# Optimization experiments

Hardware: AMD Instinct MI355X
Metric: run time of the kernel (lower is better)

Reference implementation:

```python
import jax, jax.numpy as jnp
import numpy as np

FEATS = 1024
HEAD = 16
MLP_HIDDEN = 4096
B, N = 8, 1024
EPS = 1e-5


def _layernorm(x, g, b):
    mu = jnp.mean(x, axis=-1, keepdims=True)
    var = jnp.var(x, axis=-1, keepdims=True)
    return (x - mu) * jax.lax.rsqrt(var + EPS) * g + b


def setup_inputs() -> dict:
    key = jax.random.key(0)
    ks = jax.random.split(key, 12)
    s_attn = 1.0 / np.sqrt(FEATS)
    s_mlp1 = 1.0 / np.sqrt(FEATS)
    s_mlp2 = 1.0 / np.sqrt(MLP_HIDDEN)
    return {
        "x": jax.random.normal(ks[0], (B, N, FEATS), dtype=jnp.float32),
        "ln1_g": jnp.ones((FEATS,), jnp.float32),
        "ln1_b": jnp.zeros((FEATS,), jnp.float32),
        "wq": jax.random.normal(ks[1], (FEATS, FEATS), jnp.float32) * s_attn,
        "bq": jnp.zeros((FEATS,), jnp.float32),
        "wk": jax.random.normal(ks[2], (FEATS, FEATS), jnp.float32) * s_attn,
        "bk": jnp.zeros((FEATS,), jnp.float32),
        "wv": jax.random.normal(ks[3], (FEATS, FEATS), jnp.float32) * s_attn,
        "bv": jnp.zeros((FEATS,), jnp.float32),
        "wo": jax.random.normal(ks[4], (FEATS, FEATS), jnp.float32) * s_attn,
        "bo": jnp.zeros((FEATS,), jnp.float32),
        "ln2_g": jnp.ones((FEATS,), jnp.float32),
        "ln2_b": jnp.zeros((FEATS,), jnp.float32),
        "w1": jax.random.normal(ks[5], (FEATS, MLP_HIDDEN), jnp.float32) * s_mlp1,
        "b1": jnp.zeros((MLP_HIDDEN,), jnp.float32),
        "w2": jax.random.normal(ks[6], (MLP_HIDDEN, FEATS), jnp.float32) * s_mlp2,
        "b2": jnp.zeros((FEATS,), jnp.float32),
    }


def reference(x, ln1_g, ln1_b, wq, bq, wk, bk, wv, bv, wo, bo,
              ln2_g, ln2_b, w1, b1, w2, b2):
    b, n, f = x.shape
    d = f // HEAD
    sqrt_d = jnp.asarray(f, x.dtype) ** 0.5  # NOTE: scale by sqrt(feats), as in source

    h = _layernorm(x, ln1_g, ln1_b)
    # [b, n, f] -> [b, head, n, d]
    q = (h @ wq + bq).reshape(b, n, HEAD, d).transpose(0, 2, 1, 3)
    k = (h @ wk + bk).reshape(b, n, HEAD, d).transpose(0, 2, 1, 3)
    v = (h @ wv + bv).reshape(b, n, HEAD, d).transpose(0, 2, 1, 3)

    score = jnp.einsum('bhif,bhjf->bhij', q, k) / sqrt_d
    p = jax.nn.softmax(score, axis=-1)
    attn = jnp.einsum('bhij,bhjf->bihf', p, v).reshape(b, n, f)
    o = attn @ wo + bo
    out = o + x

    h2 = _layernorm(out, ln2_g, ln2_b)
    m = jax.nn.gelu(h2 @ w1 + b1, approximate=False)
    m = jax.nn.gelu(m @ w2 + b2, approximate=False)
    return m + out
```

## Files before the change

kernel.cpp:

```cpp
#include <hip/hip_runtime.h>
#include <cstdint>

typedef __bf16 bf16;
typedef __attribute__((ext_vector_type(8))) __bf16 bf16x8;
typedef __attribute__((ext_vector_type(4))) __bf16 bf16x4;
typedef __attribute__((ext_vector_type(4))) float f32x4;
typedef __attribute__((ext_vector_type(8))) unsigned short u16x8;

#define AS1C(p) ((const __attribute__((address_space(1))) void*)(p))
#define AS3(p)  ((__attribute__((address_space(3))) void*)(p))

__device__ __forceinline__ float gelu_exact(float v) {
    return 0.5f * v * (1.0f + erff(v * 0.7071067811865476f));
}

__global__ __launch_bounds__(256, 1) void wtrans_kernel(
    const float* __restrict__ w, bf16* __restrict__ wt, int K, int N)
{
    __shared__ float tile[64][65];
    const int k0 = blockIdx.y * 64, n0 = blockIdx.x * 64;
    const int tid = threadIdx.x;
    {
        const int kl = tid >> 2, nc = (tid & 3) * 16;
        #pragma unroll
        for (int i = 0; i < 4; ++i) {
            const float4 v = *(const float4*)&w[(size_t)(k0 + kl) * N + n0 + nc + i * 4];
            tile[kl][nc + i * 4 + 0] = v.x;
            tile[kl][nc + i * 4 + 1] = v.y;
            tile[kl][nc + i * 4 + 2] = v.z;
            tile[kl][nc + i * 4 + 3] = v.w;
        }
    }
    __syncthreads();
    {
        const int nl = tid >> 2, kc = (tid & 3) * 16;
        #pragma unroll
        for (int i = 0; i < 4; ++i) {
            bf16x4 o4;
            o4[0] = (bf16)tile[kc + i * 4 + 0][nl];
            o4[1] = (bf16)tile[kc + i * 4 + 1][nl];
            o4[2] = (bf16)tile[kc + i * 4 + 2][nl];
            o4[3] = (bf16)tile[kc + i * 4 + 3][nl];
            *(bf16x4*)&wt[(size_t)(n0 + nl) * K + k0 + kc + i * 4] = o4;
        }
    }
}

__global__ void bias3_kernel(const float* __restrict__ a, const float* __restrict__ b,
                             const float* __restrict__ c, float* __restrict__ o)
{
    const int i = blockIdx.x * 256 + threadIdx.x;
    o[i] = (i < 1024) ? a[i] : (i < 2048 ? b[i - 1024] : c[i - 2048]);
}

__global__ __launch_bounds__(256, 1) void ln_kernel(
    const float* __restrict__ x, const float* __restrict__ gw,
    const float* __restrict__ bw, bf16* __restrict__ out)
{
    const int row = blockIdx.x, tid = threadIdx.x;
    const float4 v = *(const float4*)&x[(size_t)row * 1024 + tid * 4];
    float s = v.x + v.y + v.z + v.w;
    float q = v.x * v.x + v.y * v.y + v.z * v.z + v.w * v.w;
    #pragma unroll
    for (int off = 32; off > 0; off >>= 1) {
        s += __shfl_xor(s, off);
        q += __shfl_xor(q, off);
    }
    __shared__ float red[8];
    if ((tid & 63) == 0) { red[tid >> 6] = s; red[4 + (tid >> 6)] = q; }
    __syncthreads();
    s = red[0] + red[1] + red[2] + red[3];
    q = red[4] + red[5] + red[6] + red[7];
    const float mu = s * (1.f / 1024.f);
    const float rs = rsqrtf(q * (1.f / 1024.f) - mu * mu + 1e-5f);
    const float4 gg = *(const float4*)&gw[tid * 4];
    const float4 bb = *(const float4*)&bw[tid * 4];
    bf16x4 o4;
    o4[0] = (bf16)((v.x - mu) * rs * gg.x + bb.x);
    o4[1] = (bf16)((v.y - mu) * rs * gg.y + bb.y);
    o4[2] = (bf16)((v.z - mu) * rs * gg.z + bb.z);
    o4[3] = (bf16)((v.w - mu) * rs * gg.w + bb.w);
    *(bf16x4*)&out[(size_t)row * 1024 + tid * 4] = o4;
}

template<int EPI>
__global__ __launch_bounds__(512, 2) void gemm_v10_kernel(
    const bf16* __restrict__ A, const bf16* __restrict__ BT,
    const float* __restrict__ bias, const float* __restrict__ res,
    void* __restrict__ out, int M, int N, int Kstride, int Klen)
{
    constexpr int ABYTES = 256 * 128;
    constexpr int BUFB = 512 * 128;
    extern __shared__ char lds[];

    const int tid = threadIdx.x;
    const int lane = tid & 63, wid = tid >> 6;
    const int wr = wid >> 2, wc = wid & 3;
    const int j = lane & 15, g = lane >> 4;
    const int skc = ((tid & 7) ^ ((tid >> 4) & 7)) << 3;

    const int nbn = N >> 8;
    const int nwg = (M >> 8) * nbn;
    const int wg = (blockIdx.x & 7) * ((int)gridDim.x >> 3) + (blockIdx.x >> 3);
    const int half = wg / nwg;
    const int wgl = wg - half * nwg;
    const int bm = (wgl / nbn) << 8;
    const int bn = (wgl % nbn) << 8;
    const int kbase = half * Klen;

    const bf16* srcA[4];
    const bf16* srcB[4];
    #pragma unroll
    for (int ga = 0; ga < 4; ++ga)
        srcA[ga] = A + (size_t)(bm + ga * 64 + (tid >> 3)) * Kstride + kbase + skc;
    #pragma unroll
    for (int gb = 0; gb < 4; ++gb)
        srcB[gb] = BT + (size_t)(bn + gb * 64 + (tid >> 3)) * Kstride + kbase + skc;

    auto stage = [&](char* obuf) {
        #pragma unroll
        for (int ga = 0; ga < 4; ++ga) {
            __builtin_amdgcn_global_load_lds(AS1C(srcA[ga]), AS3(obuf + ga * 8192 + tid * 16), 16, 0, 0);
            srcA[ga] += 64;
        }
        #pragma unroll
        for (int gb = 0; gb < 4; ++gb) {
            __builtin_amdgcn_global_load_lds(AS1C(srcB[gb]), AS3(obuf + ABYTES + gb * 8192 + tid * 16), 16, 0, 0);
            srcB[gb] += 64;
        }
    };
    auto rdA = [&](char* buf, int h, int mf, int ks) {
        const int R = wr * 128 + (h * 4 + mf) * 16 + j;
        uint32_t lb = (uint32_t)(R * 128 + ks * 64 + g * 16);
        lb ^= (lb >> 4) & 0x70u;
        return *(const bf16x8*)(buf + lb);
    };
    auto rdB = [&](char* buf, int nf, int ks) {
        const int R = wc * 64 + nf * 16 + j;
        uint32_t lb = (uint32_t)(R * 128 + ks * 64 + g * 16);
        lb ^= (lb >> 4) & 0x70u;
        return *(const bf16x8*)(buf + ABYTES + lb);
    };

    f32x4 acc[8][4] = {};
    const int NT = Klen >> 6;

    stage(lds);
    asm volatile("s_waitcnt vmcnt(0)" ::: "memory");
    __builtin_amdgcn_s_barrier();

    for (int t = 0; t < NT; ++t) {
        char* buf = lds + (t & 1) * BUFB;

        bf16x8 bfr[4][2], af[4][2];
        #pragma unroll
        for (int nf = 0; nf < 4; ++nf)
            #pragma unroll
            for (int ks = 0; ks < 2; ++ks) bfr[nf][ks] = rdB(buf, nf, ks);
        #pragma unroll
        for (int mf = 0; mf < 4; ++mf)
            #pragma unroll
            for (int ks = 0; ks < 2; ++ks) af[mf][ks] = rdA(buf, 0, mf, ks);
        if (t + 1 < NT) stage(lds + ((t + 1) & 1) * BUFB);
        __builtin_amdgcn_sched_barrier(0);
        __builtin_amdgcn_s_setprio(1);
        #pragma unroll
        for (int mf = 0; mf < 4; ++mf)
            #pragma unroll
            for (int nf = 0; nf < 4; ++nf)
                #pragma unroll
                for (int ks = 0; ks < 2; ++ks)
                    acc[mf][nf] = __builtin_amdgcn_mfma_f32_16x16x32_bf16(
                        af[mf][ks], bfr[nf][ks], acc[mf][nf], 0, 0, 0);
        __builtin_amdgcn_s_setprio(0);
        bf16x8 af1[4][2];
        #pragma unroll
        for (int mf = 0; mf < 4; ++mf)
            #pragma unroll
            for (int ks = 0; ks < 2; ++ks) af1[mf][ks] = rdA(buf, 1, mf, ks);
        __builtin_amdgcn_sched_barrier(0);
        __builtin_amdgcn_s_setprio(1);
        #pragma unroll
        for (int mf = 0; mf < 4; ++mf)
            #pragma unroll
            for (int nf = 0; nf < 4; ++nf)
                #pragma unroll
                for (int ks = 0; ks < 2; ++ks)
                    acc[4 + mf][nf] = __builtin_amdgcn_mfma_f32_16x16x32_bf16(
                        af1[mf][ks], bfr[nf][ks], acc[4 + mf][nf], 0, 0, 0);
        __builtin_amdgcn_s_setprio(0);
        asm volatile("s_waitcnt vmcnt(0)" ::: "memory");
        __builtin_amdgcn_s_barrier();
    }

    const int row0 = bm + wr * 128;
    const int col0 = bn + wc * 64;
    float* po = nullptr;
    if constexpr (EPI == 4)
        po = half ? (float*)res : (float*)out;
    #pragma unroll
    for (int nf = 0; nf < 4; ++nf) {
        const int col = col0 + nf * 16 + j;
        const float bs = (EPI == 4) ? 0.f : bias[col];
        #pragma unroll
        for (int mf = 0; mf < 8; ++mf) {
            #pragma unroll
            for (int r = 0; r < 4; ++r) {
                const int row = row0 + mf * 16 + g * 4 + r;
                float v = acc[mf][nf][r] + bs;
                if constexpr (EPI == 4) {
                    po[(size_t)row * N + col] = v;
                } else if constexpr (EPI == 2) {
                    ((bf16*)out)[(size_t)row * N + col] = (bf16)gelu_exact(v);
                } else if constexpr (EPI == 1) {
                    v += res[(size_t)row * N + col];
                    ((float*)out)[(size_t)row * N + col] = v;
                } else {
                    ((bf16*)out)[(size_t)row * N + col] = (bf16)v;
                }
            }
        }
    }
}

__global__ __launch_bounds__(256, 1) void reduce2_kernel(
    const float* __restrict__ p0, const float* __restrict__ p1,
    const float* __restrict__ bias, const float* __restrict__ res,
    float* __restrict__ out)
{
    const size_t i4 = ((size_t)blockIdx.x * 256 + threadIdx.x) * 4;
    const float4 a = *(const float4*)&p0[i4];
    const float4 b = *(const float4*)&p1[i4];
    const float4 r = *(const float4*)&res[i4];
    const float4 bs = *(const float4*)&bias[i4 & 1023];
    float4 o;
    o.x = gelu_exact(a.x + b.x + bs.x) + r.x;
    o.y = gelu_exact(a.y + b.y + bs.y) + r.y;
    o.z = gelu_exact(a.z + b.z + bs.z) + r.z;
    o.w = gelu_exact(a.w + b.w + bs.w) + r.w;
    *(float4*)&out[i4] = o;
}

__global__ __launch_bounds__(256, 1) void attn_kernel(
    const bf16* __restrict__ qkv, bf16* __restrict__ attn, int bh_base)
{
    const int tid = threadIdx.x;
    const int lane = tid & 63, wid = tid >> 6;
    const int j = lane & 15, g = lane >> 4;

    const int lin = blockIdx.x + blockIdx.y * 8;
    const int virt = (lin & 7) * 64 + (lin >> 3);
    const int bh = bh_base + (virt >> 3), qp = virt & 7;
    const int b = bh >> 4, h = bh & 15;
    const int q0a = qp * 128 + wid * 16;
    const int q0b = q0a + 64;

    const bf16* Qp = qkv + (size_t)b * 1024 * 3072 + h * 64;
    const bf16* Kp = Qp + 1024;
    const bf16* Vp = Qp + 2048;

    __shared__ __attribute__((aligned(16))) uint32_t vTu[4][64][36];

    const int kp = (tid & 31) * 2;
    const int d0 = (tid >> 5) * 8;
    #pragma unroll
    for (int pb = 0; pb < 2; ++pb) {
        const u16x8 r0 = *(const u16x8*)&Vp[(size_t)(pb * 64 + kp) * 3072 + d0];
        const u16x8 r1 = *(const u16x8*)&Vp[(size_t)(pb * 64 + kp + 1) * 3072 + d0];
        #pragma unroll
        for (int i = 0; i < 8; ++i)
            vTu[pb][d0 + i][kp >> 1] = (uint32_t)r0[i] | ((uint32_t)r1[i] << 16);
    }

    bf16x8 qa0 = *(const bf16x8*)&Qp[(size_t)(q0a + j) * 3072 + g * 8];
    bf16x8 qa1 = *(const bf16x8*)&Qp[(size_t)(q0a + j) * 3072 + 32 + g * 8];
    bf16x8 qb0 = *(const bf16x8*)&Qp[(size_t)(q0b + j) * 3072 + g * 8];
    bf16x8 qb1 = *(const bf16x8*)&Qp[(size_t)(q0b + j) * 3072 + 32 + g * 8];
    #pragma unroll
    for (int e = 0; e < 8; ++e) {
        qa0[e] = (bf16)((float)qa0[e] * 0.03125f);
        qa1[e] = (bf16)((float)qa1[e] * 0.03125f);
        qb0[e] = (bf16)((float)qb0[e] * 0.03125f);
        qb1[e] = (bf16)((float)qb1[e] * 0.03125f);
    }

    const int jperm = (j >> 2) * 8 + (j & 3);

    f32x4 oa[4] = {}, ob[4] = {};
    float mra = -1e30f, lsa = 0.f;
    float mrb = -1e30f, lsb = 0.f;

    bf16x8 kfA[4][2], kfB[4][2];
    #pragma unroll
    for (int t = 0; t < 4; ++t) {
        const int key = (t >> 1) * 32 + jperm + (t & 1) * 4;
        kfA[t][0] = *(const bf16x8*)&Kp[(size_t)key * 3072 + g * 8];
        kfA[t][1] = *(const bf16x8*)&Kp[(size_t)key * 3072 + 32 + g * 8];
    }

    asm volatile("s_waitcnt lgkmcnt(0)" ::: "memory");
    __builtin_amdgcn_s_barrier();

    auto softmax = [&](f32x4 (&s)[4], float& mrun, float& lsum, f32x4 (&o)[4]) {
        float cur = fmaxf(fmaxf(s[0][0], s[0][1]), fmaxf(s[0][2], s[0][3]));
        #pragma unroll
        for (int t = 1; t < 4; ++t)
            cur = fmaxf(cur, fmaxf(fmaxf(s[t][0], s[t][1]), fmaxf(s[t][2], s[t][3])));
        cur = fmaxf(cur, __shfl_xor(cur, 16));
        cur = fmaxf(cur, __shfl_xor(cur, 32));
        if (!__all(cur - mrun <= 8.0f)) {
            const float mnew = fmaxf(mrun, cur);
            const float alpha = __expf(mrun - mnew);
            float al[4];
            #pragma unroll
            for (int r = 0; r < 4; ++r) al[r] = __shfl(alpha, g * 4 + r);
            #pragma unroll
            for (int dt = 0; dt < 4; ++dt)
                #pragma unroll
                for (int r = 0; r < 4; ++r) o[dt][r] *= al[r];
            lsum *= alpha;
            mrun = mnew;
        }
        float ps = 0.f;
        #pragma unroll
        for (int t = 0; t < 4; ++t)
            #pragma unroll
            for (int r = 0; r < 4; ++r) {
                const float p = __expf(s[t][r] - mrun);
                s[t][r] = p;
                ps += p;
            }
        lsum += ps;
    };

    auto iter = [&](int c, bf16x8 (&kf)[4][2], bf16x8 (&kfn)[4][2]) {
        const f32x4 zero = {0.f, 0.f, 0.f, 0.f};
        const bool pfv = (c + 2 < 16);
        const bool pfk = (c + 1 < 16);

        u16x8 r0, r1;
        if (pfv) {
            const size_t vb = (size_t)((c + 2) * 64 + kp) * 3072 + d0;
            r0 = *(const u16x8*)&Vp[vb];
            r1 = *(const u16x8*)&Vp[vb + 3072];
        }

        f32x4 sa[4], sb[4];
        #pragma unroll
        for (int t = 0; t < 4; ++t) {
            sa[t] = __builtin_amdgcn_mfma_f32_16x16x32_bf16(kf[t][0], qa0, zero, 0, 0, 0);
            sb[t] = __builtin_amdgcn_mfma_f32_16x16x32_bf16(kf[t][0], qb0, zero, 0, 0, 0);
            sa[t] = __builtin_amdgcn_mfma_f32_16x16x32_bf16(kf[t][1], qa1, sa[t], 0, 0, 0);
            sb[t] = __builtin_amdgcn_mfma_f32_16x16x32_bf16(kf[t][1], qb1, sb[t], 0, 0, 0);
        }

        if (pfk) {
            #pragma unroll
            for (int t = 0; t < 4; ++t) {
                const int key = (c + 1) * 64 + (t >> 1) * 32 + jperm + (t & 1) * 4;
                kfn[t][0] = *(const bf16x8*)&Kp[(size_t)key * 3072 + g * 8];
                kfn[t][1] = *(const bf16x8*)&Kp[(size_t)key * 3072 + 32 + g * 8];
            }
        }

        softmax(sa, mra, lsa, oa);
        softmax(sb, mrb, lsb, ob);

        bf16x8 paa0, paa1, pab0, pab1;
        #pragma unroll
        for (int r = 0; r < 4; ++r) {
            paa0[r]     = (bf16)sa[0][r];
            paa0[4 + r] = (bf16)sa[1][r];
            paa1[r]     = (bf16)sa[2][r];
            paa1[4 + r] = (bf16)sa[3][r];
            pab0[r]     = (bf16)sb[0][r];
            pab0[4 + r] = (bf16)sb[1][r];
            pab1[r]     = (bf16)sb[2][r];
            pab1[4 + r] = (bf16)sb[3][r];
        }

        if (pfv) {
            const int wb = (c + 2) & 3;
            #pragma unroll
            for (int i = 0; i < 8; ++i)
                vTu[wb][d0 + i][kp >> 1] = (uint32_t)r0[i] | ((uint32_t)r1[i] << 16);
        }

        const int rb = c & 3;
        #pragma unroll
        for (int dt = 0; dt < 4; ++dt) {
            const bf16* vrow = (const bf16*)&vTu[rb][dt * 16 + j][0];
            const bf16x8 vb0 = *(const bf16x8*)(vrow + g * 8);
            const bf16x8 vb1 = *(const bf16x8*)(vrow + 32 + g * 8);
            oa[dt] = __builtin_amdgcn_mfma_f32_16x16x32_bf16(paa0, vb0, oa[dt], 0, 0, 0);
            ob[dt] = __builtin_amdgcn_mfma_f32_16x16x32_bf16(pab0, vb0, ob[dt], 0, 0, 0);
            oa[dt] = __builtin_amdgcn_mfma_f32_16x16x32_bf16(paa1, vb1, oa[dt], 0, 0, 0);
            ob[dt] = __builtin_amdgcn_mfma_f32_16x16x32_bf16(pab1, vb1, ob[dt], 0, 0, 0);
        }
    };

    for (int cc = 0; cc < 16; cc += 2) {
        iter(cc,     kfA, kfB);
        iter(cc + 1, kfB, kfA);
        asm volatile("s_waitcnt lgkmcnt(0)" ::: "memory");
        __builtin_amdgcn_sched_barrier(0);
        __builtin_amdgcn_s_barrier();
    }

    lsa += __shfl_xor(lsa, 16);
    lsa += __shfl_xor(lsa, 32);
    lsb += __shfl_xor(lsb, 16);
    lsb += __shfl_xor(lsb, 32);
    float inva[4], invb[4];
    #pragma unroll
    for (int r = 0; r < 4; ++r) {
        inva[r] = 1.0f / __shfl(lsa, g * 4 + r);
        invb[r] = 1.0f / __shfl(lsb, g * 4 + r);
    }
    #pragma unroll
    for (int dt = 0; dt < 4; ++dt)
        #pragma unroll
        for (int r = 0; r < 4; ++r) {
            attn[(size_t)(b * 1024 + q0a + g * 4 + r) * 1024 + h * 64 + dt * 16 + j] =
                (bf16)(oa[dt][r] * inva[r]);
            attn[(size_t)(b * 1024 + q0b + g * 4 + r) * 1024 + h * 64 + dt * 16 + j] =
                (bf16)(ob[dt][r] * invb[r]);
        }
}

extern "C" void kernel_launch(void* const* d_in, const int* in_sizes, int n_in,
                              void* d_out, int out_size, void* d_ws, size_t ws_size,
                              hipStream_t stream)
{
    const float* x    = (const float*)d_in[0];
    const float* ln1g = (const float*)d_in[1];
    const float* ln1b = (const float*)d_in[2];
    const float* wq   = (const float*)d_in[3];
    const float* bq   = (const float*)d_in[4];
    const float* wk   = (const float*)d_in[5];
    const float* bk   = (const float*)d_in[6];
    const float* wv   = (const float*)d_in[7];
    const float* bv   = (const float*)d_in[8];
    const float* wo   = (const float*)d_in[9];
    const float* bo   = (const float*)d_in[10];
    const float* ln2g = (const float*)d_in[11];
    const float* ln2b = (const float*)d_in[12];
    const float* w1   = (const float*)d_in[13];
    const float* b1   = (const float*)d_in[14];
    const float* w2   = (const float*)d_in[15];
    const float* b2   = (const float*)d_in[16];

    char* ws = (char*)d_ws;
    bf16* wqkvT = (bf16*)ws;  ws += (size_t)3072 * 1024 * 2;
    bf16* woT   = (bf16*)ws;  ws += (size_t)1024 * 1024 * 2;
    bf16* w1T   = (bf16*)ws;  ws += (size_t)4096 * 1024 * 2;
    bf16* w2T   = (bf16*)ws;  ws += (size_t)1024 * 4096 * 2;
    float* bqkv = (float*)ws; ws += (size_t)3072 * 4;
    bf16* h     = (bf16*)ws;  ws += (size_t)8192 * 1024 * 2;
    bf16* qkv   = (bf16*)ws;  ws += (size_t)8192 * 3072 * 2;
    bf16* attn  = (bf16*)ws;  ws += (size_t)8192 * 1024 * 2;
    float* outf = (float*)ws; ws += (size_t)8192 * 1024 * 4;
    bf16* m1    = (bf16*)ws;  ws += (size_t)8192 * 4096 * 2;
    float* p1   = (float*)ws; ws += (size_t)8192 * 1024 * 4;
    float* p0   = (float*)qkv;

    (void)hipFuncSetAttribute((const void*)gemm_v10_kernel<0>,
                              hipFuncAttributeMaxDynamicSharedMemorySize, 131072);
    (void)hipFuncSetAttribute((const void*)gemm_v10_kernel<1>,
                              hipFuncAttributeMaxDynamicSharedMemorySize, 131072);
    (void)hipFuncSetAttribute((const void*)gemm_v10_kernel<2>,
                              hipFuncAttributeMaxDynamicSharedMemorySize, 131072);
    (void)hipFuncSetAttribute((const void*)gemm_v10_kernel<4>,
                              hipFuncAttributeMaxDynamicSharedMemorySize, 131072);

    wtrans_kernel<<<dim3(16, 16), 256, 0, stream>>>(wq, wqkvT,                   1024, 1024);
    wtrans_kernel<<<dim3(16, 16), 256, 0, stream>>>(wk, wqkvT + 1024 * 1024,     1024, 1024);
    wtrans_kernel<<<dim3(16, 16), 256, 0, stream>>>(wv, wqkvT + 2 * 1024 * 1024, 1024, 1024);
    wtrans_kernel<<<dim3(16, 16), 256, 0, stream>>>(wo, woT, 1024, 1024);
    wtrans_kernel<<<dim3(64, 16), 256, 0, stream>>>(w1, w1T, 1024, 4096);
    wtrans_kernel<<<dim3(16, 64), 256, 0, stream>>>(w2, w2T, 4096, 1024);
    bias3_kernel<<<12, 256, 0, stream>>>(bq, bk, bv, bqkv);

    ln_kernel<<<8192, 256, 0, stream>>>(x, ln1g, ln1b, h);
    gemm_v10_kernel<0><<<384, 512, 131072, stream>>>(h, wqkvT, bqkv, nullptr, qkv, 8192, 3072, 1024, 1024);
    attn_kernel<<<dim3(8, 64), 256, 0, stream>>>(qkv, attn, 0);
    attn_kernel<<<dim3(8, 64), 256, 0, stream>>>(qkv, attn, 64);
    gemm_v10_kernel<1><<<128, 512, 131072, stream>>>(attn, woT, bo, x, outf, 8192, 1024, 1024, 1024);
    ln_kernel<<<8192, 256, 0, stream>>>(outf, ln2g, ln2b, h);
    gemm_v10_kernel<2><<<512, 512, 131072, stream>>>(h, w1T, b1, nullptr, m1, 8192, 4096, 1024, 1024);
    gemm_v10_kernel<4><<<256, 512, 131072, stream>>>(m1, w2T, nullptr, p1, p0, 8192, 1024, 4096, 2048);
    reduce2_kernel<<<8192, 256, 0, stream>>>(p0, p1, b2, outf, (float*)d_out);
}
```

Baseline: 449.4 us.

## Replace 256x256 pipelined GEMM with simple 128x128 single-buffered tiles

Swaps the double-buffered 256x256-tile, 512-thread GEMM for a 128x128-tile, 256-thread kernel. It uses a K step of 32, a single LDS buffer with no swizzle, and two barriers per iteration. The output-projection GEMM now uses split-K with a separate reduction pass, the reduce kernel gains a non-GELU mode, and the other launches grow their grids to match the smaller tiles. The aim is more workgroups and higher occupancy, at the cost of losing load/compute overlap, adding LDS bank conflicts, doing less data reuse per tile, and making an extra memory pass.

```diff
diff --git a/kernel.cpp b/kernel.cpp
--- a/kernel.cpp
+++ b/kernel.cpp
@@ -84,130 +84,70 @@
 }
 
 template<int EPI>
-__global__ __launch_bounds__(512, 2) void gemm_v10_kernel(
+__global__ __launch_bounds__(256, 3) void gemm_v11_kernel(
     const bf16* __restrict__ A, const bf16* __restrict__ BT,
     const float* __restrict__ bias, const float* __restrict__ res,
     void* __restrict__ out, int M, int N, int Kstride, int Klen)
 {
-    constexpr int ABYTES = 256 * 128;
-    constexpr int BUFB = 512 * 128;
-    extern __shared__ char lds[];
-
+    __shared__ __attribute__((aligned(16))) bf16 lA[128 * 32];
+    __shared__ __attribute__((aligned(16))) bf16 lB[128 * 32];
     const int tid = threadIdx.x;
-    const int lane = tid & 63, wid = tid >> 6;
-    const int wr = wid >> 2, wc = wid & 3;
+    const int lane = tid & 63;
+    const int wid = tid >> 6;
+    const int wr = wid >> 1, wc = wid & 1;
     const int j = lane & 15, g = lane >> 4;
-    const int skc = ((tid & 7) ^ ((tid >> 4) & 7)) << 3;
-
-    const int nbn = N >> 8;
-    const int nwg = (M >> 8) * nbn;
-    const int wg = (blockIdx.x & 7) * ((int)gridDim.x >> 3) + (blockIdx.x >> 3);
+
+    const int nbn = N >> 7;
+    const int nwg = (M >> 7) * nbn;
+    const int wg = ((int)blockIdx.x & 7) * ((int)gridDim.x >> 3) + ((int)blockIdx.x >> 3);
     const int half = wg / nwg;
     const int wgl = wg - half * nwg;
-    const int bm = (wgl / nbn) << 8;
-    const int bn = (wgl % nbn) << 8;
+    const int bm = (wgl / nbn) << 7;
+    const int bn = (wgl % nbn) << 7;
     const int kbase = half * Klen;
 
-    const bf16* srcA[4];
-    const bf16* srcB[4];
-    #pragma unroll
-    for (int ga = 0; ga < 4; ++ga)
-        srcA[ga] = A + (size_t)(bm + ga * 64 + (tid >> 3)) * Kstride + kbase + skc;
-    #pragma unroll
-    for (int gb = 0; gb < 4; ++gb)
-        srcB[gb] = BT + (size_t)(bn + gb * 64 + (tid >> 3)) * Kstride + kbase + skc;
-
-    auto stage = [&](char* obuf) {
-        #pragma unroll
-        for (int ga = 0; ga < 4; ++ga) {
-            __builtin_amdgcn_global_load_lds(AS1C(srcA[ga]), AS3(obuf + ga * 8192 + tid * 16), 16, 0, 0);
-            srcA[ga] += 64;
-        }
-        #pragma unroll
-        for (int gb = 0; gb < 4; ++gb) {
-            __builtin_amdgcn_global_load_lds(AS1C(srcB[gb]), AS3(obuf + ABYTES + gb * 8192 + tid * 16), 16, 0, 0);
-            srcB[gb] += 64;
-        }
-    };
-    auto rdA = [&](char* buf, int h, int mf, int ks) {
-        const int R = wr * 128 + (h * 4 + mf) * 16 + j;
-        uint32_t lb = (uint32_t)(R * 128 + ks * 64 + g * 16);
-        lb ^= (lb >> 4) & 0x70u;
-        return *(const bf16x8*)(buf + lb);
-    };
-    auto rdB = [&](char* buf, int nf, int ks) {
-        const int R = wc * 64 + nf * 16 + j;
-        uint32_t lb = (uint32_t)(R * 128 + ks * 64 + g * 16);
-        lb ^= (lb >> 4) & 0x70u;
-        return *(const bf16x8*)(buf + ABYTES + lb);
-    };
-
-    f32x4 acc[8][4] = {};
-    const int NT = Klen >> 6;
-
-    stage(lds);
-    asm volatile("s_waitcnt vmcnt(0)" ::: "memory");
-    __builtin_amdgcn_s_barrier();
-
-    for (int t = 0; t < NT; ++t) {
-        char* buf = lds + (t & 1) * BUFB;
-
-        bf16x8 bfr[4][2], af[4][2];
-        #pragma unroll
-        for (int nf = 0; nf < 4; ++nf)
-            #pragma unroll
-            for (int ks = 0; ks < 2; ++ks) bfr[nf][ks] = rdB(buf, nf, ks);
-        #pragma unroll
-        for (int mf = 0; mf < 4; ++mf)
-            #pragma unroll
-            for (int ks = 0; ks < 2; ++ks) af[mf][ks] = rdA(buf, 0, mf, ks);
-        if (t + 1 < NT) stage(lds + ((t + 1) & 1) * BUFB);
-        __builtin_amdgcn_sched_barrier(0);
-        __builtin_amdgcn_s_setprio(1);
-        #pragma unroll
-        for (int mf = 0; mf < 4; ++mf)
-            #pragma unroll
-            for (int nf = 0; nf < 4; ++nf)
-                #pragma unroll
-                for (int ks = 0; ks < 2; ++ks)
-                    acc[mf][nf] = __builtin_amdgcn_mfma_f32_16x16x32_bf16(
-                        af[mf][ks], bfr[nf][ks], acc[mf][nf], 0, 0, 0);
-        __builtin_amdgcn_s_setprio(0);
-        bf16x8 af1[4][2];
-        #pragma unroll
-        for (int mf = 0; mf < 4; ++mf)
-            #pragma unroll
-            for (int ks = 0; ks < 2; ++ks) af1[mf][ks] = rdA(buf, 1, mf, ks);
-        __builtin_amdgcn_sched_barrier(0);
-        __builtin_amdgcn_s_setprio(1);
-        #pragma unroll
-        for (int mf = 0; mf < 4; ++mf)
-            #pragma unroll
-            for (int nf = 0; nf < 4; ++nf)
-                #pragma unroll
-                for (int ks = 0; ks < 2; ++ks)
-                    acc[4 + mf][nf] = __builtin_amdgcn_mfma_f32_16x16x32_bf16(
-                        af1[mf][ks], bfr[nf][ks], acc[4 + mf][nf], 0, 0, 0);
-        __builtin_amdgcn_s_setprio(0);
-        asm volatile("s_waitcnt vmcnt(0)" ::: "memory");
-        __builtin_amdgcn_s_barrier();
-    }
-
-    const int row0 = bm + wr * 128;
+    f32x4 acc[4][4] = {};
+
+    for (int k0 = 0; k0 < Klen; k0 += 32) {
+        #pragma unroll
+        for (int L = 0; L < 2; ++L) {
+            const int c = L * 256 + tid;
+            const bf16* ga = A + (size_t)(bm + (c >> 2)) * Kstride + kbase + k0 + ((c & 3) << 3);
+            __builtin_amdgcn_global_load_lds(AS1C(ga), AS3(lA + (L * 256 + wid * 64) * 8), 16, 0, 0);
+            const bf16* gb = BT + (size_t)(bn + (c >> 2)) * Kstride + kbase + k0 + ((c & 3) << 3);
+            __builtin_amdgcn_global_load_lds(AS1C(gb), AS3(lB + (L * 256 + wid * 64) * 8), 16, 0, 0);
+        }
+        __syncthreads();
+        bf16x8 af[4], bfr[4];
+        #pragma unroll
+        for (int m = 0; m < 4; ++m)
+            af[m] = *(const bf16x8*)&lA[(wr * 64 + m * 16 + j) * 32 + g * 8];
+        #pragma unroll
+        for (int n = 0; n < 4; ++n)
+            bfr[n] = *(const bf16x8*)&lB[(wc * 64 + n * 16 + j) * 32 + g * 8];
+        #pragma unroll
+        for (int m = 0; m < 4; ++m)
+            #pragma unroll
+            for (int n = 0; n < 4; ++n)
+                acc[m][n] = __builtin_amdgcn_mfma_f32_16x16x32_bf16(af[m], bfr[n], acc[m][n], 0, 0, 0);
+        __syncthreads();
+    }
+
+    const int row0 = bm + wr * 64;
     const int col0 = bn + wc * 64;
     float* po = nullptr;
     if constexpr (EPI == 4)
         po = half ? (float*)res : (float*)out;
     #pragma unroll
-    for (int nf = 0; nf < 4; ++nf) {
-        const int col = col0 + nf * 16 + j;
+    for (int n = 0; n < 4; ++n) {
+        const int col = col0 + n * 16 + j;
         const float bs = (EPI == 4) ? 0.f : bias[col];
         #pragma unroll
-        for (int mf = 0; mf < 8; ++mf) {
+        for (int m = 0; m < 4; ++m) {
             #pragma unroll
             for (int r = 0; r < 4; ++r) {
-                const int row = row0 + mf * 16 + g * 4 + r;
-                float v = acc[mf][nf][r] + bs;
+                const int row = row0 + m * 16 + g * 4 + r;
+                float v = acc[m][n][r] + bs;
                 if constexpr (EPI == 4) {
                     po[(size_t)row * N + col] = v;
                 } else if constexpr (EPI == 2) {
@@ -223,6 +163,7 @@
     }
 }
 
+template<int GELU>
 __global__ __launch_bounds__(256, 1) void reduce2_kernel(
     const float* __restrict__ p0, const float* __restrict__ p1,
     const float* __restrict__ bias, const float* __restrict__ res,
@@ -234,10 +175,17 @@
     const float4 r = *(const float4*)&res[i4];
     const float4 bs = *(const float4*)&bias[i4 & 1023];
     float4 o;
-    o.x = gelu_exact(a.x + b.x + bs.x) + r.x;
-    o.y = gelu_exact(a.y + b.y + bs.y) + r.y;
-    o.z = gelu_exact(a.z + b.z + bs.z) + r.z;
-    o.w = gelu_exact(a.w + b.w + bs.w) + r.w;
+    if constexpr (GELU) {
+        o.x = gelu_exact(a.x + b.x + bs.x) + r.x;
+        o.y = gelu_exact(a.y + b.y + bs.y) + r.y;
+        o.z = gelu_exact(a.z + b.z + bs.z) + r.z;
+        o.w = gelu_exact(a.w + b.w + bs.w) + r.w;
+    } else {
+        o.x = a.x + b.x + bs.x + r.x;
+        o.y = a.y + b.y + bs.y + r.y;
+        o.z = a.z + b.z + bs.z + r.z;
+        o.w = a.w + b.w + bs.w + r.w;
+    }
     *(float4*)&out[i4] = o;
 }
 
@@ -464,15 +412,6 @@
     float* p1   = (float*)ws; ws += (size_t)8192 * 1024 * 4;
     float* p0   = (float*)qkv;
 
-    (void)hipFuncSetAttribute((const void*)gemm_v10_kernel<0>,
-                              hipFuncAttributeMaxDynamicSharedMemorySize, 131072);
-    (void)hipFuncSetAttribute((const void*)gemm_v10_kernel<1>,
-                              hipFuncAttributeMaxDynamicSharedMemorySize, 131072);
-    (void)hipFuncSetAttribute((const void*)gemm_v10_kernel<2>,
-                              hipFuncAttributeMaxDynamicSharedMemorySize, 131072);
-    (void)hipFuncSetAttribute((const void*)gemm_v10_kernel<4>,
-                              hipFuncAttributeMaxDynamicSharedMemorySize, 131072);
-
     wtrans_kernel<<<dim3(16, 16), 256, 0, stream>>>(wq, wqkvT,                   1024, 1024);
     wtrans_kernel<<<dim3(16, 16), 256, 0, stream>>>(wk, wqkvT + 1024 * 1024,     1024, 1024);
     wtrans_kernel<<<dim3(16, 16), 256, 0, stream>>>(wv, wqkvT + 2 * 1024 * 1024, 1024, 1024);
@@ -482,12 +421,13 @@
     bias3_kernel<<<12, 256, 0, stream>>>(bq, bk, bv, bqkv);
 
     ln_kernel<<<8192, 256, 0, stream>>>(x, ln1g, ln1b, h);
-    gemm_v10_kernel<0><<<384, 512, 131072, stream>>>(h, wqkvT, bqkv, nullptr, qkv, 8192, 3072, 1024, 1024);
+    gemm_v11_kernel<0><<<1536, 256, 0, stream>>>(h, wqkvT, bqkv, nullptr, qkv, 8192, 3072, 1024, 1024);
     attn_kernel<<<dim3(8, 64), 256, 0, stream>>>(qkv, attn, 0);
     attn_kernel<<<dim3(8, 64), 256, 0, stream>>>(qkv, attn, 64);
-    gemm_v10_kernel<1><<<128, 512, 131072, stream>>>(attn, woT, bo, x, outf, 8192, 1024, 1024, 1024);
+    gemm_v11_kernel<4><<<1024, 256, 0, stream>>>(attn, woT, nullptr, p1, p0, 8192, 1024, 1024, 512);
+    reduce2_kernel<0><<<8192, 256, 0, stream>>>(p0, p1, bo, x, outf);
     ln_kernel<<<8192, 256, 0, stream>>>(outf, ln2g, ln2b, h);
-    gemm_v10_kernel<2><<<512, 512, 131072, stream>>>(h, w1T, b1, nullptr, m1, 8192, 4096, 1024, 1024);
-    gemm_v10_kernel<4><<<256, 512, 131072, stream>>>(m1, w2T, nullptr, p1, p0, 8192, 1024, 4096, 2048);
-    reduce2_kernel<<<8192, 256, 0, stream>>>(p0, p1, b2, outf, (float*)d_out);
-}
+    gemm_v11_kernel<2><<<2048, 256, 0, stream>>>(h, w1T, b1, nullptr, m1, 8192, 4096, 1024, 1024);
+    gemm_v11_kernel<4><<<1024, 256, 0, stream>>>(m1, w2T, nullptr, p1, p0, 8192, 1024, 4096, 2048);
+    reduce2_kernel<1><<<8192, 256, 0, stream>>>(p0, p1, b2, outf, (float*)d_out);
+}
```

New measurement: 466.5 us. +3.8%, slower.

## Interleave GEMM prefetch in quarter stages; split-K the output projection; merge attention launches

Applied to the files above, without the earlier changes.

The GEMM main loop now splits each K-tile into four MFMA quadrants. It issues the next tile's global-to-LDS loads in halves between them, with partial vmcnt waits and extra barriers, so loads overlap compute more finely. The attention output projection becomes a split-K GEMM (256 WGs instead of 128) followed by a reduce kernel that adds bias and residual, improving occupancy on the smaller GEMM. The two attention launches are merged into one grid. The costs are more barriers per iteration and an extra fp32 partial round trip for the projection.

```diff
diff --git a/kernel.cpp b/kernel.cpp
--- a/kernel.cpp
+++ b/kernel.cpp
@@ -84,7 +84,7 @@
 }
 
 template<int EPI>
-__global__ __launch_bounds__(512, 2) void gemm_v10_kernel(
+__global__ __launch_bounds__(512, 2) void gemm_v12_kernel(
     const bf16* __restrict__ A, const bf16* __restrict__ BT,
     const float* __restrict__ bias, const float* __restrict__ res,
     void* __restrict__ out, int M, int N, int Kstride, int Klen)
@@ -117,14 +117,18 @@
     for (int gb = 0; gb < 4; ++gb)
         srcB[gb] = BT + (size_t)(bn + gb * 64 + (tid >> 3)) * Kstride + kbase + skc;
 
-    auto stage = [&](char* obuf) {
-        #pragma unroll
-        for (int ga = 0; ga < 4; ++ga) {
+    auto stageA2 = [&](char* obuf, int first) {
+        #pragma unroll
+        for (int q = 0; q < 2; ++q) {
+            const int ga = first + q * 2;
             __builtin_amdgcn_global_load_lds(AS1C(srcA[ga]), AS3(obuf + ga * 8192 + tid * 16), 16, 0, 0);
             srcA[ga] += 64;
         }
-        #pragma unroll
-        for (int gb = 0; gb < 4; ++gb) {
+    };
+    auto stageB2 = [&](char* obuf, int first) {
+        #pragma unroll
+        for (int q = 0; q < 2; ++q) {
+            const int gb = first + q;
             __builtin_amdgcn_global_load_lds(AS1C(srcB[gb]), AS3(obuf + ABYTES + gb * 8192 + tid * 16), 16, 0, 0);
             srcB[gb] += 64;
         }
@@ -145,51 +149,101 @@
     f32x4 acc[8][4] = {};
     const int NT = Klen >> 6;
 
-    stage(lds);
-    asm volatile("s_waitcnt vmcnt(0)" ::: "memory");
+    stageA2(lds, 0);
+    stageB2(lds, 0);
+    stageB2(lds, 2);
+    stageA2(lds, 1);
+    asm volatile("s_waitcnt vmcnt(2)" ::: "memory");
     __builtin_amdgcn_s_barrier();
 
     for (int t = 0; t < NT; ++t) {
-        char* buf = lds + (t & 1) * BUFB;
-
-        bf16x8 bfr[4][2], af[4][2];
-        #pragma unroll
-        for (int nf = 0; nf < 4; ++nf)
-            #pragma unroll
-            for (int ks = 0; ks < 2; ++ks) bfr[nf][ks] = rdB(buf, nf, ks);
+        char* buf  = lds + (t & 1) * BUFB;
+        char* nbuf = lds + ((t + 1) & 1) * BUFB;
+        const bool pf = (t + 1 < NT);
+
+        bf16x8 a0[4][2], b0[2][2];
         #pragma unroll
         for (int mf = 0; mf < 4; ++mf)
             #pragma unroll
-            for (int ks = 0; ks < 2; ++ks) af[mf][ks] = rdA(buf, 0, mf, ks);
-        if (t + 1 < NT) stage(lds + ((t + 1) & 1) * BUFB);
+            for (int ks = 0; ks < 2; ++ks) a0[mf][ks] = rdA(buf, 0, mf, ks);
+        #pragma unroll
+        for (int nf = 0; nf < 2; ++nf)
+            #pragma unroll
+            for (int ks = 0; ks < 2; ++ks) b0[nf][ks] = rdB(buf, nf, ks);
+        if (pf) stageA2(nbuf, 0);
+        __builtin_amdgcn_s_barrier();
+        asm volatile("s_waitcnt lgkmcnt(0)" ::: "memory");
         __builtin_amdgcn_sched_barrier(0);
         __builtin_amdgcn_s_setprio(1);
         #pragma unroll
         for (int mf = 0; mf < 4; ++mf)
             #pragma unroll
-            for (int nf = 0; nf < 4; ++nf)
+            for (int nf = 0; nf < 2; ++nf)
                 #pragma unroll
                 for (int ks = 0; ks < 2; ++ks)
                     acc[mf][nf] = __builtin_amdgcn_mfma_f32_16x16x32_bf16(
-                        af[mf][ks], bfr[nf][ks], acc[mf][nf], 0, 0, 0);
+                        a0[mf][ks], b0[nf][ks], acc[mf][nf], 0, 0, 0);
         __builtin_amdgcn_s_setprio(0);
-        bf16x8 af1[4][2];
-        #pragma unroll
-        for (int mf = 0; mf < 4; ++mf)
-            #pragma unroll
-            for (int ks = 0; ks < 2; ++ks) af1[mf][ks] = rdA(buf, 1, mf, ks);
+        __builtin_amdgcn_s_barrier();
+
+        bf16x8 b1[2][2];
+        #pragma unroll
+        for (int nf = 0; nf < 2; ++nf)
+            #pragma unroll
+            for (int ks = 0; ks < 2; ++ks) b1[nf][ks] = rdB(buf, 2 + nf, ks);
+        if (pf) stageB2(nbuf, 0);
+        __builtin_amdgcn_s_barrier();
+        asm volatile("s_waitcnt lgkmcnt(0)" ::: "memory");
         __builtin_amdgcn_sched_barrier(0);
         __builtin_amdgcn_s_setprio(1);
         #pragma unroll
         for (int mf = 0; mf < 4; ++mf)
             #pragma unroll
-            for (int nf = 0; nf < 4; ++nf)
+            for (int nf = 0; nf < 2; ++nf)
+                #pragma unroll
+                for (int ks = 0; ks < 2; ++ks)
+                    acc[mf][2 + nf] = __builtin_amdgcn_mfma_f32_16x16x32_bf16(
+                        a0[mf][ks], b1[nf][ks], acc[mf][2 + nf], 0, 0, 0);
+        __builtin_amdgcn_s_setprio(0);
+        if (pf) asm volatile("s_waitcnt vmcnt(4)" ::: "memory");
+        else    asm volatile("s_waitcnt vmcnt(0)" ::: "memory");
+        __builtin_amdgcn_s_barrier();
+
+        bf16x8 a1[4][2];
+        #pragma unroll
+        for (int mf = 0; mf < 4; ++mf)
+            #pragma unroll
+            for (int ks = 0; ks < 2; ++ks) a1[mf][ks] = rdA(buf, 1, mf, ks);
+        if (pf) stageB2(nbuf, 2);
+        __builtin_amdgcn_s_barrier();
+        asm volatile("s_waitcnt lgkmcnt(0)" ::: "memory");
+        __builtin_amdgcn_sched_barrier(0);
+        __builtin_amdgcn_s_setprio(1);
+        #pragma unroll
+        for (int mf = 0; mf < 4; ++mf)
+            #pragma unroll
+            for (int nf = 0; nf < 2; ++nf)
                 #pragma unroll
                 for (int ks = 0; ks < 2; ++ks)
                     acc[4 + mf][nf] = __builtin_amdgcn_mfma_f32_16x16x32_bf16(
-                        af1[mf][ks], bfr[nf][ks], acc[4 + mf][nf], 0, 0, 0);
+                        a1[mf][ks], b0[nf][ks], acc[4 + mf][nf], 0, 0, 0);
         __builtin_amdgcn_s_setprio(0);
-        asm volatile("s_waitcnt vmcnt(0)" ::: "memory");
+        __builtin_amdgcn_s_barrier();
+
+        if (pf) stageA2(nbuf, 1);
+        __builtin_amdgcn_s_barrier();
+        __builtin_amdgcn_sched_barrier(0);
+        __builtin_amdgcn_s_setprio(1);
+        #pragma unroll
+        for (int mf = 0; mf < 4; ++mf)
+            #pragma unroll
+            for (int nf = 0; nf < 2; ++nf)
+                #pragma unroll
+                for (int ks = 0; ks < 2; ++ks)
+                    acc[4 + mf][2 + nf] = __builtin_amdgcn_mfma_f32_16x16x32_bf16(
+                        a1[mf][ks], b1[nf][ks], acc[4 + mf][2 + nf], 0, 0, 0);
+        __builtin_amdgcn_s_setprio(0);
+        if (pf) asm volatile("s_waitcnt vmcnt(2)" ::: "memory");
         __builtin_amdgcn_s_barrier();
     }
 
@@ -212,9 +266,6 @@
                     po[(size_t)row * N + col] = v;
                 } else if constexpr (EPI == 2) {
                     ((bf16*)out)[(size_t)row * N + col] = (bf16)gelu_exact(v);
-                } else if constexpr (EPI == 1) {
-                    v += res[(size_t)row * N + col];
-                    ((float*)out)[(size_t)row * N + col] = v;
                 } else {
                     ((bf16*)out)[(size_t)row * N + col] = (bf16)v;
                 }
@@ -223,6 +274,7 @@
     }
 }
 
+template<int GELU>
 __global__ __launch_bounds__(256, 1) void reduce2_kernel(
     const float* __restrict__ p0, const float* __restrict__ p1,
     const float* __restrict__ bias, const float* __restrict__ res,
@@ -234,23 +286,30 @@
     const float4 r = *(const float4*)&res[i4];
     const float4 bs = *(const float4*)&bias[i4 & 1023];
     float4 o;
-    o.x = gelu_exact(a.x + b.x + bs.x) + r.x;
-    o.y = gelu_exact(a.y + b.y + bs.y) + r.y;
-    o.z = gelu_exact(a.z + b.z + bs.z) + r.z;
-    o.w = gelu_exact(a.w + b.w + bs.w) + r.w;
+    if constexpr (GELU) {
+        o.x = gelu_exact(a.x + b.x + bs.x) + r.x;
+        o.y = gelu_exact(a.y + b.y + bs.y) + r.y;
+        o.z = gelu_exact(a.z + b.z + bs.z) + r.z;
+        o.w = gelu_exact(a.w + b.w + bs.w) + r.w;
+    } else {
+        o.x = a.x + b.x + bs.x + r.x;
+        o.y = a.y + b.y + bs.y + r.y;
+        o.z = a.z + b.z + bs.z + r.z;
+        o.w = a.w + b.w + bs.w + r.w;
+    }
     *(float4*)&out[i4] = o;
 }
 
 __global__ __launch_bounds__(256, 1) void attn_kernel(
-    const bf16* __restrict__ qkv, bf16* __restrict__ attn, int bh_base)
+    const bf16* __restrict__ qkv, bf16* __restrict__ attn)
 {
     const int tid = threadIdx.x;
     const int lane = tid & 63, wid = tid >> 6;
     const int j = lane & 15, g = lane >> 4;
 
     const int lin = blockIdx.x + blockIdx.y * 8;
-    const int virt = (lin & 7) * 64 + (lin >> 3);
-    const int bh = bh_base + (virt >> 3), qp = virt & 7;
+    const int virt = (lin & 7) * 128 + (lin >> 3);
+    const int bh = virt >> 3, qp = virt & 7;
     const int b = bh >> 4, h = bh & 15;
     const int q0a = qp * 128 + wid * 16;
     const int q0b = q0a + 64;
@@ -464,13 +523,11 @@
     float* p1   = (float*)ws; ws += (size_t)8192 * 1024 * 4;
     float* p0   = (float*)qkv;
 
-    (void)hipFuncSetAttribute((const void*)gemm_v10_kernel<0>,
+    (void)hipFuncSetAttribute((const void*)gemm_v12_kernel<0>,
                               hipFuncAttributeMaxDynamicSharedMemorySize, 131072);
-    (void)hipFuncSetAttribute((const void*)gemm_v10_kernel<1>,
+    (void)hipFuncSetAttribute((const void*)gemm_v12_kernel<2>,
                               hipFuncAttributeMaxDynamicSharedMemorySize, 131072);
-    (void)hipFuncSetAttribute((const void*)gemm_v10_kernel<2>,
-                              hipFuncAttributeMaxDynamicSharedMemorySize, 131072);
-    (void)hipFuncSetAttribute((const void*)gemm_v10_kernel<4>,
+    (void)hipFuncSetAttribute((const void*)gemm_v12_kernel<4>,
                               hipFuncAttributeMaxDynamicSharedMemorySize, 131072);
 
     wtrans_kernel<<<dim3(16, 16), 256, 0, stream>>>(wq, wqkvT,                   1024, 1024);
@@ -482,12 +539,12 @@
     bias3_kernel<<<12, 256, 0, stream>>>(bq, bk, bv, bqkv);
 
     ln_kernel<<<8192, 256, 0, stream>>>(x, ln1g, ln1b, h);
-    gemm_v10_kernel<0><<<384, 512, 131072, stream>>>(h, wqkvT, bqkv, nullptr, qkv, 8192, 3072, 1024, 1024);
-    attn_kernel<<<dim3(8, 64), 256, 0, stream>>>(qkv, attn, 0);
-    attn_kernel<<<dim3(8, 64), 256, 0, stream>>>(qkv, attn, 64);
-    gemm_v10_kernel<1><<<128, 512, 131072, stream>>>(attn, woT, bo, x, outf, 8192, 1024, 1024, 1024);
+    gemm_v12_kernel<0><<<384, 512, 131072, stream>>>(h, wqkvT, bqkv, nullptr, qkv, 8192, 3072, 1024, 1024);
+    attn_kernel<<<dim3(8, 128), 256, 0, stream>>>(qkv, attn);
+    gemm_v12_kernel<4><<<256, 512, 131072, stream>>>(attn, woT, nullptr, p1, p0, 8192, 1024, 1024, 512);
+    reduce2_kernel<0><<<8192, 256, 0, stream>>>(p0, p1, bo, x, outf);
     ln_kernel<<<8192, 256, 0, stream>>>(outf, ln2g, ln2b, h);
-    gemm_v10_kernel<2><<<512, 512, 131072, stream>>>(h, w1T, b1, nullptr, m1, 8192, 4096, 1024, 1024);
-    gemm_v10_kernel<4><<<256, 512, 131072, stream>>>(m1, w2T, nullptr, p1, p0, 8192, 1024, 4096, 2048);
-    reduce2_kernel<<<8192, 256, 0, stream>>>(p0, p1, b2, outf, (float*)d_out);
-}
+    gemm_v12_kernel<2><<<512, 512, 131072, stream>>>(h, w1T, b1, nullptr, m1, 8192, 4096, 1024, 1024);
+    gemm_v12_kernel<4><<<256, 512, 131072, stream>>>(m1, w2T, nullptr, p1, p0, 8192, 1024, 4096, 2048);
+    reduce2_kernel<1><<<8192, 256, 0, stream>>>(p0, p1, b2, outf, (float*)d_out);
+}
```

Result: slower. 463.5 us (+3.1%).
